# Kernel optimization log

Measured on AMD Instinct MI355X. Metric: run time of the kernel, lower is better.

The kernel has to match this reference:

```python
import jax, jax.numpy as jnp
import numpy as np

D = 1280          # hidden_size
NH = 16           # num_heads
HD = 80           # head_dim
DEPTH = 4         # number of vision blocks
INTER = 3420      # mlp intermediate size
MERGE = 2         # spatial_merge_size
OUT = 3584        # merger out_hidden_size
GRID = (1, 40, 40)  # (t, h, w) patch grid -> 1600 tokens
N = GRID[0] * GRID[1] * GRID[2]
PATCH_IN = 3 * 2 * 14 * 14  # in_channels * temporal_patch * patch^2 = 1176


def _pos_emb():
    """Deterministic vision RoPE cos/sin per Qwen2_5_VLVisionModel.rot_pos_emb."""
    t, h, w = GRID
    mh, mw = h // MERGE, w // MERGE
    intra = np.arange(MERGE)
    row = np.arange(mh)[:, None, None, None] * MERGE + intra[None, None, :, None]
    col = np.arange(mw)[None, :, None, None] * MERGE + intra[None, None, None, :]
    row = np.broadcast_to(row, (mh, mw, MERGE, MERGE)).reshape(-1)
    col = np.broadcast_to(col, (mh, mw, MERGE, MERGE)).reshape(-1)
    pos = np.stack([row, col], axis=-1)        # (h*w, 2)
    if t > 1:
        pos = np.tile(pos, (t, 1))
    rot_dim = HD // 2                          # 40
    inv = 1.0 / (10000.0 ** (np.arange(0, rot_dim, 2, dtype=np.float64) / rot_dim))
    table = np.outer(np.arange(max(h, w)), inv)        # (max_hw, rot_dim//2)
    rpe = table[pos].reshape(pos.shape[0], -1)         # (N, rot_dim)
    emb = np.concatenate([rpe, rpe], axis=-1)          # (N, HD)
    return np.cos(emb).astype(np.float32), np.sin(emb).astype(np.float32)


def setup_inputs() -> dict:
    key = jax.random.key(0)
    ks = iter(jax.random.split(key, 40))
    def w(shape, s=0.02):
        return jax.random.normal(next(ks), shape, jnp.float32) * s
    cos, sin = _pos_emb()
    return dict(
        pixel_values=w((N, PATCH_IN), 1.0),
        cos=jnp.asarray(cos), sin=jnp.asarray(sin),
        patch_w=w((D, PATCH_IN)),                       # Conv3d stride==kernel -> linear
        norm1_w=jnp.ones((DEPTH, D), jnp.float32),
        qkv_w=w((DEPTH, 3 * D, D)), qkv_b=jnp.zeros((DEPTH, 3 * D), jnp.float32),
        proj_w=w((DEPTH, D, D)), proj_b=jnp.zeros((DEPTH, D), jnp.float32),
        norm2_w=jnp.ones((DEPTH, D), jnp.float32),
        gate_w=w((DEPTH, INTER, D)), gate_b=jnp.zeros((DEPTH, INTER), jnp.float32),
        up_w=w((DEPTH, INTER, D)), up_b=jnp.zeros((DEPTH, INTER), jnp.float32),
        down_w=w((DEPTH, D, INTER)), down_b=jnp.zeros((DEPTH, D), jnp.float32),
        lnq_w=jnp.ones((D,), jnp.float32),
        m1_w=w((D * MERGE ** 2, D * MERGE ** 2)), m1_b=jnp.zeros((D * MERGE ** 2,), jnp.float32),
        m2_w=w((OUT, D * MERGE ** 2)), m2_b=jnp.zeros((OUT,), jnp.float32),
    )


def _rms(x, w, eps=1e-6):
    return x * jax.lax.rsqrt(jnp.mean(x * x, axis=-1, keepdims=True) + eps) * w


def _rotate_half(x):
    x1, x2 = jnp.split(x, 2, axis=-1)
    return jnp.concatenate([-x2, x1], axis=-1)


def _forward(pixel_values, cos, sin, patch_w, norm1_w, qkv_w, qkv_b, proj_w, proj_b,
             norm2_w, gate_w, gate_b, up_w, up_b, down_w, down_b,
             lnq_w, m1_w, m1_b, m2_w, m2_b):
    # patch embed: Conv3d with kernel==stride collapses to a linear projection
    x = pixel_values @ patch_w.T                       # (N, D)
    c = cos[:, None, :]                                # (N, 1, HD)
    s = sin[:, None, :]
    scale = HD ** -0.5
    for i in range(DEPTH):
        # --- attention ---
        h = _rms(x, norm1_w[i])
        qkv = (h @ qkv_w[i].T + qkv_b[i]).reshape(N, 3, NH, HD)
        q, k, v = qkv[:, 0], qkv[:, 1], qkv[:, 2]      # (N, NH, HD)
        q = q * c + _rotate_half(q) * s
        k = k * c + _rotate_half(k) * s
        # NOTE: this impl applies NO cu_seqlens window mask -> full dense attention
        aw = jnp.einsum('nhd,mhd->hnm', q, k) * scale  # (NH, N, N)
        aw = jax.nn.softmax(aw.astype(jnp.float32), axis=-1).astype(x.dtype)
        o = jnp.einsum('hnm,mhd->nhd', aw, v).reshape(N, D)
        x = x + o @ proj_w[i].T + proj_b[i]
        # --- mlp (SwiGLU) ---
        h = _rms(x, norm2_w[i])
        g = h @ gate_w[i].T + gate_b[i]
        u = h @ up_w[i].T + up_b[i]
        x = x + (jax.nn.silu(g) * u) @ down_w[i].T + down_b[i]
    # --- patch merger ---
    h = _rms(x, lnq_w).reshape(-1, D * MERGE ** 2)      # (N/4, 5120)
    h = jax.nn.gelu(h @ m1_w.T + m1_b, approximate=False)
    return h @ m2_w.T + m2_b                            # (N/4, OUT)


def reference(pixel_values, cos, sin, patch_w, norm1_w, qkv_w, qkv_b, proj_w, proj_b,
              norm2_w, gate_w, gate_b, up_w, up_b, down_w, down_b,
              lnq_w, m1_w, m1_b, m2_w, m2_b):
    return _forward(pixel_values, cos, sin, patch_w, norm1_w, qkv_w, qkv_b, proj_w,
                    proj_b, norm2_w, gate_w, gate_b, up_w, up_b, down_w, down_b,
                    lnq_w, m1_w, m1_b, m2_w, m2_b)
```

## Files before the change

### kernel.cpp

```cpp
#include <hip/hip_runtime.h>


typedef __bf16 bf16x8 __attribute__((ext_vector_type(8)));
typedef float  f32x4  __attribute__((ext_vector_type(4)));
typedef unsigned short u16;

#define DEV __device__ __forceinline__

DEV u16 f2bf(float f) {
    union { float f; unsigned u; } v; v.f = f;
    unsigned r = v.u + 0x7FFFu + ((v.u >> 16) & 1u);
    return (u16)(r >> 16);
}
DEV float bf2f(u16 b) {
    union { float f; unsigned u; } v; v.u = ((unsigned)b) << 16; return v.f;
}

DEV void gload16(const u16* g, u16* l) {
    __builtin_amdgcn_global_load_lds(
        (const __attribute__((address_space(1))) unsigned int*)g,
        (__attribute__((address_space(3))) unsigned int*)l, 16, 0, 0);
}

enum { EPI_NONE = 0, EPI_BIAS = 1, EPI_BIAS_RESID = 2, EPI_BIAS_GELU = 3, EPI_PART = 4 };

DEV unsigned xcd_map(unsigned lin, unsigned nwg) {
    unsigned q = nwg >> 3, r = nwg & 7, xc = lin & 7, off = lin >> 3;
    return (xc < r ? xc * (q + 1) : r * (q + 1) + (xc - r) * q) + off;
}

__global__ void cvt_kernel(const float* __restrict__ src, u16* __restrict__ dst,
                           int Rs, int Cs, int Rp, int Cp,
                           long long sls, long long dls)
{
    const float* s = src + (size_t)blockIdx.y * sls;
    u16* d = dst + (size_t)blockIdx.y * dls;
    int idx = blockIdx.x * 256 + threadIdx.x;
    int cpc = Cp >> 3;
    if (idx >= Rp * cpc) return;
    int row = idx / cpc;
    int c0  = (idx - row * cpc) * 8;
    u16 v[8];
    if (row < Rs && c0 + 8 <= Cs) {
        float4 a = *reinterpret_cast<const float4*>(&s[(size_t)row * Cs + c0]);
        float4 b = *reinterpret_cast<const float4*>(&s[(size_t)row * Cs + c0 + 4]);
        v[0] = f2bf(a.x); v[1] = f2bf(a.y); v[2] = f2bf(a.z); v[3] = f2bf(a.w);
        v[4] = f2bf(b.x); v[5] = f2bf(b.y); v[6] = f2bf(b.z); v[7] = f2bf(b.w);
    } else {
#pragma unroll
        for (int j = 0; j < 8; ++j) {
            int c = c0 + j;
            v[j] = (row < Rs && c < Cs) ? f2bf(s[(size_t)row * Cs + c]) : (u16)0;
        }
    }
    *reinterpret_cast<uint4*>(&d[(size_t)row * Cp + c0]) =
        *reinterpret_cast<const uint4*>(v);
}

__global__ void gub_kernel(const float* __restrict__ gb, const float* __restrict__ ub,
                           float* __restrict__ dst)
{
    int i = blockIdx.x * 256 + threadIdx.x;
    if (i >= 4 * 6912) return;
    int l = i / 6912, c = i - l * 6912;
    float v = 0.f;
    if (c < 3456) { if (c < 3420) v = gb[l * 3420 + c]; }
    else { int c2 = c - 3456; if (c2 < 3420) v = ub[l * 3420 + c2]; }
    dst[i] = v;
}

template <int EPI, bool OF32>
__global__ __launch_bounds__(256, 3)
void gemm16_kernel(const u16* __restrict__ A, const u16* __restrict__ B,
                   const float* __restrict__ bias, const float* __restrict__ resid,
                   void* __restrict__ outp, int Kp, int ldc, int Rlim,
                   int ktn, size_t zstride)
{
    __shared__ u16 sA[3][4096];
    __shared__ u16 sB[3][4096];
    const int tid  = threadIdx.x;
    const int lane = tid & 63;
    const int w    = tid >> 6;

    const unsigned gy  = gridDim.y;
    const unsigned nwg = gridDim.x * gy;
    const unsigned lin = blockIdx.x + blockIdx.y * gridDim.x;
    const unsigned id2 = xcd_map(lin, nwg);
    const int c0 = (int)(id2 / gy) * 128;
    const int r0 = (int)(id2 - (id2 / gy) * gy) * 128;

    const int wr  = (w >> 1) * 64;
    const int wc  = (w & 1) * 64;
    const int l15 = lane & 15;
    const int kk  = (lane >> 4) * 8;
    const int pco = (((lane >> 4) ^ ((l15 >> 1) & 3)) * 8) - kk;

    const int ca  = w * 128 + lane;
    const int cb  = ca + 64;
    const int sza = ((ca & 3) ^ ((ca >> 3) & 3)) * 8;
    const int szb = ((cb & 3) ^ ((cb >> 3) & 3)) * 8;
    const size_t arow0 = (size_t)(r0 + (ca >> 2)) * Kp + sza;
    const size_t brow0 = (size_t)(c0 + (ca >> 2)) * Kp + sza;
    const size_t arow1 = (size_t)(r0 + (cb >> 2)) * Kp + szb;
    const size_t brow1 = (size_t)(c0 + (cb >> 2)) * Kp + szb;

    f32x4 acc[4][4];
#pragma unroll
    for (int i = 0; i < 4; ++i)
#pragma unroll
        for (int j = 0; j < 4; ++j) acc[i][j] = (f32x4){0.f, 0.f, 0.f, 0.f};

    const int kt0 = blockIdx.z * ktn;
    auto stage = [&](int kt, int buf) {
        int k0 = kt * 32;
        gload16(A + arow0 + k0, &sA[buf][ca * 8]);
        gload16(B + brow0 + k0, &sB[buf][ca * 8]);
        gload16(A + arow1 + k0, &sA[buf][cb * 8]);
        gload16(B + brow1 + k0, &sB[buf][cb * 8]);
    };
    auto compute = [&](int buf) {
        bf16x8 af[4], bfr[4];
#pragma unroll
        for (int f = 0; f < 4; ++f) {
            af[f]  = *reinterpret_cast<const bf16x8*>(&sA[buf][(wr + f * 16 + l15) * 32 + kk + pco]);
            bfr[f] = *reinterpret_cast<const bf16x8*>(&sB[buf][(wc + f * 16 + l15) * 32 + kk + pco]);
        }
#pragma unroll
        for (int fr = 0; fr < 4; ++fr)
#pragma unroll
            for (int fc = 0; fc < 4; ++fc)
                acc[fr][fc] = __builtin_amdgcn_mfma_f32_16x16x32_bf16(af[fr], bfr[fc], acc[fr][fc], 0, 0, 0);
    };

    const int NT = ktn;
    stage(kt0, 0);
    if (NT > 1) stage(kt0 + 1, 1);
    int bcur = 0;
    for (int t = 0; t < NT - 1; ++t) {
        asm volatile("s_waitcnt vmcnt(4)" ::: "memory");
        __builtin_amdgcn_s_barrier();
        __builtin_amdgcn_sched_barrier(0);
        if (t + 2 < NT) {
            int bn = bcur + 2; if (bn >= 3) bn -= 3;
            stage(kt0 + t + 2, bn);
        }
        __builtin_amdgcn_sched_barrier(0);
        compute(bcur);
        bcur = (bcur == 2) ? 0 : bcur + 1;
    }
    asm volatile("s_waitcnt vmcnt(0)" ::: "memory");
    __builtin_amdgcn_s_barrier();
    __builtin_amdgcn_sched_barrier(0);
    compute(bcur);

    const int rowb = r0 + wr + (lane >> 4) * 4;
    const int colb = c0 + wc + l15;
    if (EPI == EPI_PART) {
        float* pp = (float*)outp + (size_t)blockIdx.z * zstride;
#pragma unroll
        for (int fc = 0; fc < 4; ++fc) {
            int col = colb + fc * 16;
#pragma unroll
            for (int fr = 0; fr < 4; ++fr)
#pragma unroll
                for (int r2 = 0; r2 < 4; ++r2)
                    pp[(size_t)(rowb + fr * 16 + r2) * ldc + col] = acc[fr][fc][r2];
        }
        return;
    }
#pragma unroll
    for (int fc = 0; fc < 4; ++fc) {
        int col = colb + fc * 16;
        float bv = (EPI != EPI_NONE) ? bias[col] : 0.f;
#pragma unroll
        for (int fr = 0; fr < 4; ++fr) {
#pragma unroll
            for (int r2 = 0; r2 < 4; ++r2) {
                int row = rowb + fr * 16 + r2;
                if (row >= Rlim) continue;
                float v = acc[fr][fc][r2] + bv;
                if (EPI == EPI_BIAS_RESID) v += resid[(size_t)row * ldc + col];
                if (EPI == EPI_BIAS_GELU)  v = 0.5f * v * (1.f + erff(v * 0.70710678118f));
                if (OF32) ((float*)outp)[(size_t)row * ldc + col] = v;
                else      ((u16*)outp)[(size_t)row * ldc + col] = f2bf(v);
            }
        }
    }
}

template <int EPI, bool OF32>
__global__ __launch_bounds__(256, 4)
void gemm64_kernel(const u16* __restrict__ A, const u16* __restrict__ B,
                   const float* __restrict__ bias, const float* __restrict__ resid,
                   void* __restrict__ outp, int Kp, int ldc, int Rlim)
{
    __shared__ u16 sA[3][2048];
    __shared__ u16 sB[3][4096];
    const int tid  = threadIdx.x;
    const int lane = tid & 63;
    const int w    = tid >> 6;

    const unsigned gy  = gridDim.y;
    const unsigned nwg = gridDim.x * gy;
    const unsigned lin = blockIdx.x + blockIdx.y * gridDim.x;
    const unsigned id2 = xcd_map(lin, nwg);
    const int c0 = (int)(id2 / gy) * 128;
    const int r0 = (int)(id2 - (id2 / gy) * gy) * 64;

    const int wr  = (w >> 1) * 32;
    const int wc  = (w & 1) * 64;
    const int l15 = lane & 15;
    const int kk  = (lane >> 4) * 8;
    const int pco = (((lane >> 4) ^ ((l15 >> 1) & 3)) * 8) - kk;

    const int cB0 = tid, cB1 = tid + 256, cA = tid;
    const size_t bsrc0 = (size_t)(c0 + (cB0 >> 2)) * Kp + ((cB0 & 3) ^ ((cB0 >> 3) & 3)) * 8;
    const size_t bsrc1 = (size_t)(c0 + (cB1 >> 2)) * Kp + ((cB1 & 3) ^ ((cB1 >> 3) & 3)) * 8;
    const size_t asrc  = (size_t)(r0 + (cA  >> 2)) * Kp + ((cA  & 3) ^ ((cA  >> 3) & 3)) * 8;

    f32x4 acc[2][4];
#pragma unroll
    for (int i = 0; i < 2; ++i)
#pragma unroll
        for (int j = 0; j < 4; ++j) acc[i][j] = (f32x4){0.f, 0.f, 0.f, 0.f};

    auto stage = [&](int kt, int buf) {
        int k0 = kt * 32;
        gload16(B + bsrc0 + k0, &sB[buf][cB0 * 8]);
        gload16(B + bsrc1 + k0, &sB[buf][cB1 * 8]);
        gload16(A + asrc  + k0, &sA[buf][cA * 8]);
    };
    auto compute = [&](int buf) {
        bf16x8 af[2], bfr[4];
#pragma unroll
        for (int f = 0; f < 2; ++f)
            af[f]  = *reinterpret_cast<const bf16x8*>(&sA[buf][(wr + f * 16 + l15) * 32 + kk + pco]);
#pragma unroll
        for (int f = 0; f < 4; ++f)
            bfr[f] = *reinterpret_cast<const bf16x8*>(&sB[buf][(wc + f * 16 + l15) * 32 + kk + pco]);
#pragma unroll
        for (int fr = 0; fr < 2; ++fr)
#pragma unroll
            for (int fc = 0; fc < 4; ++fc)
                acc[fr][fc] = __builtin_amdgcn_mfma_f32_16x16x32_bf16(af[fr], bfr[fc], acc[fr][fc], 0, 0, 0);
    };

    const int NT = Kp >> 5;
    stage(0, 0);
    stage(1, 1);
    int bcur = 0;
    for (int t = 0; t < NT - 1; ++t) {
        asm volatile("s_waitcnt vmcnt(3)" ::: "memory");
        __builtin_amdgcn_s_barrier();
        __builtin_amdgcn_sched_barrier(0);
        if (t + 2 < NT) {
            int bn = bcur + 2; if (bn >= 3) bn -= 3;
            stage(t + 2, bn);
        }
        __builtin_amdgcn_sched_barrier(0);
        compute(bcur);
        bcur = (bcur == 2) ? 0 : bcur + 1;
    }
    asm volatile("s_waitcnt vmcnt(0)" ::: "memory");
    __builtin_amdgcn_s_barrier();
    __builtin_amdgcn_sched_barrier(0);
    compute(bcur);

    const int rowb = r0 + wr + (lane >> 4) * 4;
    const int colb = c0 + wc + l15;
#pragma unroll
    for (int fc = 0; fc < 4; ++fc) {
        int col = colb + fc * 16;
        float bv = (EPI != EPI_NONE) ? bias[col] : 0.f;
#pragma unroll
        for (int fr = 0; fr < 2; ++fr) {
#pragma unroll
            for (int r2 = 0; r2 < 4; ++r2) {
                int row = rowb + fr * 16 + r2;
                if (row >= Rlim) continue;
                float v = acc[fr][fc][r2] + bv;
                if (EPI == EPI_BIAS_RESID) v += resid[(size_t)row * ldc + col];
                if (EPI == EPI_BIAS_GELU)  v = 0.5f * v * (1.f + erff(v * 0.70710678118f));
                if (OF32) ((float*)outp)[(size_t)row * ldc + col] = v;
                else      ((u16*)outp)[(size_t)row * ldc + col] = f2bf(v);
            }
        }
    }
}

template <int EPI, bool OF32>
__global__ __launch_bounds__(256, 4)
void gemm32_kernel(const u16* __restrict__ A, const u16* __restrict__ B,
                   const float* __restrict__ bias, const float* __restrict__ resid,
                   void* __restrict__ outp, int Kp, int ldc, int Rlim)
{
    __shared__ u16 sA[3][1024];
    __shared__ u16 sB[3][4096];
    const int tid  = threadIdx.x;
    const int lane = tid & 63;
    const int w    = tid >> 6;

    const unsigned gy  = gridDim.y;
    const unsigned nwg = gridDim.x * gy;
    const unsigned lin = blockIdx.x + blockIdx.y * gridDim.x;
    const unsigned id2 = xcd_map(lin, nwg);
    const int c0 = (int)(id2 / gy) * 128;
    const int r0 = (int)(id2 - (id2 / gy) * gy) * 32;

    const int wc  = w * 32;
    const int l15 = lane & 15;
    const int kk  = (lane >> 4) * 8;
    const int pco = (((lane >> 4) ^ ((l15 >> 1) & 3)) * 8) - kk;

    const int cB0 = tid, cB1 = tid + 256, cA = tid & 127;
    const size_t bsrc0 = (size_t)(c0 + (cB0 >> 2)) * Kp + ((cB0 & 3) ^ ((cB0 >> 3) & 3)) * 8;
    const size_t bsrc1 = (size_t)(c0 + (cB1 >> 2)) * Kp + ((cB1 & 3) ^ ((cB1 >> 3) & 3)) * 8;
    const size_t asrc  = (size_t)(r0 + (cA  >> 2)) * Kp + ((cA  & 3) ^ ((cA  >> 3) & 3)) * 8;

    f32x4 acc[2][2];
#pragma unroll
    for (int i = 0; i < 2; ++i)
#pragma unroll
        for (int j = 0; j < 2; ++j) acc[i][j] = (f32x4){0.f, 0.f, 0.f, 0.f};

    auto stage = [&](int kt, int buf) {
        int k0 = kt * 32;
        gload16(B + bsrc0 + k0, &sB[buf][cB0 * 8]);
        gload16(B + bsrc1 + k0, &sB[buf][cB1 * 8]);
        gload16(A + asrc  + k0, &sA[buf][cA * 8]);
    };
    auto compute = [&](int buf) {
        bf16x8 af[2], bfr[2];
#pragma unroll
        for (int f = 0; f < 2; ++f) {
            af[f]  = *reinterpret_cast<const bf16x8*>(&sA[buf][(f * 16 + l15) * 32 + kk + pco]);
            bfr[f] = *reinterpret_cast<const bf16x8*>(&sB[buf][(wc + f * 16 + l15) * 32 + kk + pco]);
        }
#pragma unroll
        for (int fr = 0; fr < 2; ++fr)
#pragma unroll
            for (int fc = 0; fc < 2; ++fc)
                acc[fr][fc] = __builtin_amdgcn_mfma_f32_16x16x32_bf16(af[fr], bfr[fc], acc[fr][fc], 0, 0, 0);
    };

    const int NT = Kp >> 5;
    stage(0, 0);
    stage(1, 1);
    int bcur = 0;
    for (int t = 0; t < NT - 1; ++t) {
        asm volatile("s_waitcnt vmcnt(3)" ::: "memory");
        __builtin_amdgcn_s_barrier();
        __builtin_amdgcn_sched_barrier(0);
        if (t + 2 < NT) {
            int bn = bcur + 2; if (bn >= 3) bn -= 3;
            stage(t + 2, bn);
        }
        __builtin_amdgcn_sched_barrier(0);
        compute(bcur);
        bcur = (bcur == 2) ? 0 : bcur + 1;
    }
    asm volatile("s_waitcnt vmcnt(0)" ::: "memory");
    __builtin_amdgcn_s_barrier();
    __builtin_amdgcn_sched_barrier(0);
    compute(bcur);

    const int rowb = r0 + (lane >> 4) * 4;
    const int colb = c0 + wc + l15;
#pragma unroll
    for (int fc = 0; fc < 2; ++fc) {
        int col = colb + fc * 16;
        float bv = (EPI != EPI_NONE) ? bias[col] : 0.f;
#pragma unroll
        for (int fr = 0; fr < 2; ++fr) {
#pragma unroll
            for (int r2 = 0; r2 < 4; ++r2) {
                int row = rowb + fr * 16 + r2;
                if (row >= Rlim) continue;
                float v = acc[fr][fc][r2] + bv;
                if (EPI == EPI_BIAS_RESID) v += resid[(size_t)row * ldc + col];
                if (EPI == EPI_BIAS_GELU)  v = 0.5f * v * (1.f + erff(v * 0.70710678118f));
                if (OF32) ((float*)outp)[(size_t)row * ldc + col] = v;
                else      ((u16*)outp)[(size_t)row * ldc + col] = f2bf(v);
            }
        }
    }
}

template <int GELU, bool OF32>
__global__ void reduce_kernel(const float* __restrict__ part, const float* __restrict__ bias,
                              void* __restrict__ outp, int C, int S, size_t zstride, int total4)
{
    int i = blockIdx.x * 256 + threadIdx.x;
    if (i >= total4) return;
    int cq = C >> 2;
    int rr = i / cq;
    int cc = (i - rr * cq) * 4;
    size_t bidx = (size_t)rr * C + cc;
    float4 s = *reinterpret_cast<const float4*>(&part[bidx]);
    for (int z = 1; z < S; ++z) {
        float4 p = *reinterpret_cast<const float4*>(&part[z * zstride + bidx]);
        s.x += p.x; s.y += p.y; s.z += p.z; s.w += p.w;
    }
    float4 b = *reinterpret_cast<const float4*>(&bias[cc]);
    s.x += b.x; s.y += b.y; s.z += b.z; s.w += b.w;
    if (GELU) {
        s.x = 0.5f * s.x * (1.f + erff(s.x * 0.70710678118f));
        s.y = 0.5f * s.y * (1.f + erff(s.y * 0.70710678118f));
        s.z = 0.5f * s.z * (1.f + erff(s.z * 0.70710678118f));
        s.w = 0.5f * s.w * (1.f + erff(s.w * 0.70710678118f));
    }
    if (OF32) {
        *reinterpret_cast<float4*>(&((float*)outp)[bidx]) = s;
    } else {
        u16 v[4] = { f2bf(s.x), f2bf(s.y), f2bf(s.z), f2bf(s.w) };
        *reinterpret_cast<uint2*>(&((u16*)outp)[bidx]) = *reinterpret_cast<const uint2*>(v);
    }
}

__global__ void rms_kernel(const float* __restrict__ x, const float* __restrict__ w,
                           u16* __restrict__ out, int cols)
{
    const int row = blockIdx.x;
    const int tid = threadIdx.x;
    const float* xr = x + (size_t)row * cols;
    float ss = 0.f;
    for (int c = tid; c < cols; c += 256) { float v = xr[c]; ss += v * v; }
#pragma unroll
    for (int m = 1; m < 64; m <<= 1) ss += __shfl_xor(ss, m);
    __shared__ float wsum[4];
    if ((tid & 63) == 0) wsum[tid >> 6] = ss;
    __syncthreads();
    float tot = wsum[0] + wsum[1] + wsum[2] + wsum[3];
    float rs = rsqrtf(tot / (float)cols + 1e-6f);
    u16* orow = out + (size_t)row * cols;
    for (int c = tid; c < cols; c += 256) orow[c] = f2bf(xr[c] * rs * w[c]);
}

__global__ void rope_kernel(u16* __restrict__ qkv, const float* __restrict__ cosb,
                            const float* __restrict__ sinb)
{
    int idx = blockIdx.x * 256 + threadIdx.x;
    int n   = idx / 640;
    int rem = idx - n * 640;
    int hh  = rem / 40;
    int d   = rem - hh * 40;
    float c0 = cosb[n * 80 + d];
    float s0 = sinb[n * 80 + d];
    float c1 = cosb[n * 80 + d + 40];
    float s1 = sinb[n * 80 + d + 40];
    size_t base = (size_t)n * 3840 + hh * 80;
    float a = bf2f(qkv[base + d]), b = bf2f(qkv[base + d + 40]);
    qkv[base + d]      = f2bf(a * c0 - b * s0);
    qkv[base + d + 40] = f2bf(b * c1 + a * s1);
    base += 1280;
    a = bf2f(qkv[base + d]); b = bf2f(qkv[base + d + 40]);
    qkv[base + d]      = f2bf(a * c0 - b * s0);
    qkv[base + d + 40] = f2bf(b * c1 + a * s1);
}

__global__ void silu_mul_kernel(const u16* __restrict__ gu, u16* __restrict__ outb)
{
    int idx = blockIdx.x * 256 + threadIdx.x;
    if (idx >= 1664 * 432) return;
    int row = idx / 432, c8 = (idx - row * 432) * 8;
    u16 gv[8], uv[8];
    *reinterpret_cast<uint4*>(gv) = *reinterpret_cast<const uint4*>(&gu[(size_t)row * 6912 + c8]);
    *reinterpret_cast<uint4*>(uv) = *reinterpret_cast<const uint4*>(&gu[(size_t)row * 6912 + 3456 + c8]);
#pragma unroll
    for (int j = 0; j < 8; ++j) {
        float x = bf2f(gv[j]);
        gv[j] = f2bf(x / (1.f + __expf(-x)) * bf2f(uv[j]));
    }
    *reinterpret_cast<uint4*>(&outb[(size_t)row * 3456 + c8]) = *reinterpret_cast<const uint4*>(gv);
}

__global__ __launch_bounds__(256, 2)
void attn_kernel(const u16* __restrict__ qkv, u16* __restrict__ o)
{
    __shared__ __align__(16) u16      Klds[2][64][104];
    __shared__ __align__(16) unsigned Vt32[2][80][36];
    __shared__ __align__(16) u16      Plds[4][16][72];
    const int tid  = threadIdx.x;
    const int lane = tid & 63;
    const int w    = tid >> 6;
    const int l15  = lane & 15;
    const int kk   = (lane >> 4) * 8;
    unsigned lin = blockIdx.y * 25 + blockIdx.x;
    unsigned id2 = (lin & 7) * 50 + (lin >> 3);
    const int hh = (int)(id2 / 25);
    const int qt = (int)(id2 - hh * 25);
    const float scale = 0.11180339887498949f;

    const int koff = 1280 + hh * 80;
    const int voff = 2560 + hh * 80;

    {
        int r  = tid >> 2;
        int cq = 80 + (tid & 3) * 4;
        *reinterpret_cast<uint2*>(&Klds[0][r][cq]) = make_uint2(0u, 0u);
        *reinterpret_cast<uint2*>(&Klds[1][r][cq]) = make_uint2(0u, 0u);
    }

    const int qrow = qt * 64 + w * 16 + l15;
    bf16x8 aq[3];
#pragma unroll
    for (int s = 0; s < 3; ++s) {
        int d = 32 * s + kk;
        union { bf16x8 v; uint4 q; } uu;
        if (d < 80) uu.q = *reinterpret_cast<const uint4*>(&qkv[(size_t)qrow * 3840 + hh * 80 + d]);
        else        uu.q = make_uint4(0u, 0u, 0u, 0u);
        aq[s] = uu.v;
    }

    const int kc0 = tid, kc1 = tid + 256, kc2 = tid + 512;
    const int kr0 = kc0 / 10, k80 = (kc0 - kr0 * 10) * 8;
    const int kr1 = kc1 / 10, k81 = (kc1 - kr1 * 10) * 8;
    const int kr2 = kc2 / 10, k82 = (kc2 - kr2 * 10) * 8;
    const size_t ksrc0 = (size_t)kr0 * 3840 + koff + k80;
    const size_t ksrc1 = (size_t)kr1 * 3840 + koff + k81;
    const size_t ksrc2 = (size_t)kr2 * 3840 + koff + k82;
    const int rpA = tid & 31, gA = tid >> 5;
    const int gB = 8 + (tid >> 5);
    const size_t vsrcA = (size_t)(2 * rpA) * 3840 + voff + gA * 8;
    const size_t vsrcB = (size_t)(2 * rpA) * 3840 + voff + gB * 8;

    uint4 kg0, kg1, kg2, va0, va1, vb0, vb1;
    auto LOADR = [&](int kb) {
        size_t tb = (size_t)kb * 245760;
        kg0 = *reinterpret_cast<const uint4*>(&qkv[tb + ksrc0]);
        kg1 = *reinterpret_cast<const uint4*>(&qkv[tb + ksrc1]);
        if (tid < 128) kg2 = *reinterpret_cast<const uint4*>(&qkv[tb + ksrc2]);
        va0 = *reinterpret_cast<const uint4*>(&qkv[tb + vsrcA]);
        va1 = *reinterpret_cast<const uint4*>(&qkv[tb + vsrcA + 3840]);
        if (tid < 64) {
            vb0 = *reinterpret_cast<const uint4*>(&qkv[tb + vsrcB]);
            vb1 = *reinterpret_cast<const uint4*>(&qkv[tb + vsrcB + 3840]);
        }
    };
    auto STORE = [&](int b) {
        *reinterpret_cast<uint4*>(&Klds[b][kr0][k80]) = kg0;
        *reinterpret_cast<uint4*>(&Klds[b][kr1][k81]) = kg1;
        if (tid < 128) *reinterpret_cast<uint4*>(&Klds[b][kr2][k82]) = kg2;
        union { uint4 q; u16 h[8]; } xa0, xa1;
        xa0.q = va0; xa1.q = va1;
#pragma unroll
        for (int j = 0; j < 8; ++j)
            Vt32[b][gA * 8 + j][rpA] = (unsigned)xa0.h[j] | ((unsigned)xa1.h[j] << 16);
        if (tid < 64) {
            union { uint4 q; u16 h[8]; } xb0, xb1;
            xb0.q = vb0; xb1.q = vb1;
#pragma unroll
            for (int j = 0; j < 8; ++j)
                Vt32[b][gB * 8 + j][rpA] = (unsigned)xb0.h[j] | ((unsigned)xb1.h[j] << 16);
        }
    };

    f32x4 acc_o[5];
#pragma unroll
    for (int fd = 0; fd < 5; ++fd) acc_o[fd] = (f32x4){0.f, 0.f, 0.f, 0.f};
    float m[4], lsum[4];
#pragma unroll
    for (int r2 = 0; r2 < 4; ++r2) { m[r2] = -__builtin_inff(); lsum[r2] = 0.f; }

    LOADR(0);
    STORE(0);
    __syncthreads();
    int cur = 0;

    for (int kb = 0; kb < 25; ++kb) {
        if (kb < 24) LOADR(kb + 1);

        f32x4 sf[4];
#pragma unroll
        for (int fc = 0; fc < 4; ++fc) {
            f32x4 c = (f32x4){0.f, 0.f, 0.f, 0.f};
#pragma unroll
            for (int s = 0; s < 3; ++s)
                c = __builtin_amdgcn_mfma_f32_16x16x32_bf16(
                        aq[s],
                        *reinterpret_cast<const bf16x8*>(&Klds[cur][fc * 16 + l15][32 * s + kk]),
                        c, 0, 0, 0);
            sf[fc] = c * scale;
        }

        float mx[4];
#pragma unroll
        for (int r2 = 0; r2 < 4; ++r2)
            mx[r2] = fmaxf(fmaxf(sf[0][r2], sf[1][r2]), fmaxf(sf[2][r2], sf[3][r2]));
#pragma unroll
        for (int msk = 1; msk <= 8; msk <<= 1)
#pragma unroll
            for (int r2 = 0; r2 < 4; ++r2)
                mx[r2] = fmaxf(mx[r2], __shfl_xor(mx[r2], msk));
        float alpha[4];
#pragma unroll
        for (int r2 = 0; r2 < 4; ++r2) {
            float mn = fmaxf(m[r2], mx[r2]);
            alpha[r2] = __expf(m[r2] - mn);
            m[r2] = mn;
        }
        float psum[4] = {0.f, 0.f, 0.f, 0.f};
#pragma unroll
        for (int fc = 0; fc < 4; ++fc)
#pragma unroll
            for (int r2 = 0; r2 < 4; ++r2) {
                float p = __expf(sf[fc][r2] - m[r2]);
                sf[fc][r2] = p;
                psum[r2] += p;
            }
#pragma unroll
        for (int msk = 1; msk <= 8; msk <<= 1)
#pragma unroll
            for (int r2 = 0; r2 < 4; ++r2) psum[r2] += __shfl_xor(psum[r2], msk);
#pragma unroll
        for (int r2 = 0; r2 < 4; ++r2) lsum[r2] = lsum[r2] * alpha[r2] + psum[r2];
#pragma unroll
        for (int fd = 0; fd < 5; ++fd)
#pragma unroll
            for (int r2 = 0; r2 < 4; ++r2) acc_o[fd][r2] *= alpha[r2];

        const int prow = (lane >> 4) * 4;
#pragma unroll
        for (int fc = 0; fc < 4; ++fc)
#pragma unroll
            for (int r2 = 0; r2 < 4; ++r2)
                Plds[w][prow + r2][fc * 16 + l15] = f2bf(sf[fc][r2]);

        bf16x8 ap[2];
#pragma unroll
        for (int ks = 0; ks < 2; ++ks)
            ap[ks] = *reinterpret_cast<const bf16x8*>(&Plds[w][l15][32 * ks + kk]);
#pragma unroll
        for (int fd = 0; fd < 5; ++fd) {
            const u16* vrow = reinterpret_cast<const u16*>(&Vt32[cur][fd * 16 + l15][0]);
#pragma unroll
            for (int ks = 0; ks < 2; ++ks)
                acc_o[fd] = __builtin_amdgcn_mfma_f32_16x16x32_bf16(
                        ap[ks],
                        *reinterpret_cast<const bf16x8*>(&vrow[32 * ks + kk]),
                        acc_o[fd], 0, 0, 0);
        }

        if (kb < 24) STORE(cur ^ 1);
        __syncthreads();
        cur ^= 1;
    }

    float inv[4];
#pragma unroll
    for (int r2 = 0; r2 < 4; ++r2) inv[r2] = 1.f / lsum[r2];
    const int orow = qt * 64 + w * 16 + (lane >> 4) * 4;
    const int ocol = hh * 80 + l15;
#pragma unroll
    for (int fd = 0; fd < 5; ++fd)
#pragma unroll
        for (int r2 = 0; r2 < 4; ++r2)
            o[(size_t)(orow + r2) * 1280 + ocol + fd * 16] = f2bf(acc_o[fd][r2] * inv[r2]);
}

extern "C" void kernel_launch(void* const* d_in, const int* in_sizes, int n_in,
                              void* d_out, int out_size, void* d_ws, size_t ws_size,
                              hipStream_t stream)
{
    const float* pixel  = (const float*)d_in[0];
    const float* cosb   = (const float*)d_in[1];
    const float* sinb   = (const float*)d_in[2];
    const float* patchw = (const float*)d_in[3];
    const float* n1w    = (const float*)d_in[4];
    const float* qkvw   = (const float*)d_in[5];
    const float* qkvb   = (const float*)d_in[6];
    const float* projw  = (const float*)d_in[7];
    const float* projb  = (const float*)d_in[8];
    const float* n2w    = (const float*)d_in[9];
    const float* gatew  = (const float*)d_in[10];
    const float* gateb  = (const float*)d_in[11];
    const float* upw    = (const float*)d_in[12];
    const float* upb    = (const float*)d_in[13];
    const float* downw  = (const float*)d_in[14];
    const float* downb  = (const float*)d_in[15];
    const float* lnqw   = (const float*)d_in[16];
    const float* m1w    = (const float*)d_in[17];
    const float* m1b    = (const float*)d_in[18];
    const float* m2w    = (const float*)d_in[19];
    const float* m2b    = (const float*)d_in[20];
    float* out = (float*)d_out;

    char* base = (char*)d_ws;
    float* x      = (float*)(base);
    u16*   h      = (u16*)(base + 8519680);
    u16*   qbuf   = (u16*)(base + 12779520);
    u16*   pix16  = qbuf;
    u16*   gsep   = (u16*)(base + 25559040);
    u16*   o      = gsep;
    u16*   pw16   = gsep;
    u16*   gu     = (u16*)(base + 37060608);
    u16*   t1     = gu;
    float* guB    = (float*)(base + 60063744);
    u16*   qkvw16 = (u16*)(base + 60174336);
    u16*   projw16= (u16*)(base + 99495936);
    u16*   guw16  = (u16*)(base + 112603136);
    u16*   downw16= (u16*)(base + 183382016);
    u16*   m1w16  = guw16;
    u16*   m2w16  = (u16*)(base + 112603136 + 52428800);
    float* part   = (float*)qkvw16;

    dim3 blk(256);
    auto cvb = [](int Rp, int Cp) { return (Rp * (Cp >> 3) + 255) / 256; };

    cvt_kernel<<<dim3(cvb(1664,1216),1), blk, 0, stream>>>(pixel, pix16, 1600, 1176, 1664, 1216, 0, 0);
    cvt_kernel<<<dim3(cvb(1280,1216),1), blk, 0, stream>>>(patchw, pw16, 1280, 1176, 1280, 1216, 0, 0);
    cvt_kernel<<<dim3(cvb(15360,1280),1), blk, 0, stream>>>(qkvw, qkvw16, 15360, 1280, 15360, 1280, 0, 0);
    cvt_kernel<<<dim3(cvb(5120,1280),1), blk, 0, stream>>>(projw, projw16, 5120, 1280, 5120, 1280, 0, 0);
    cvt_kernel<<<dim3(cvb(3456,1280),4), blk, 0, stream>>>(gatew, guw16, 3420, 1280, 3456, 1280, 4377600LL, 8847360LL);
    cvt_kernel<<<dim3(cvb(3456,1280),4), blk, 0, stream>>>(upw, guw16 + 4423680, 3420, 1280, 3456, 1280, 4377600LL, 8847360LL);
    cvt_kernel<<<dim3(cvb(1280,3456),4), blk, 0, stream>>>(downw, downw16, 1280, 3420, 1280, 3456, 4377600LL, 4423680LL);
    gub_kernel<<<108, blk, 0, stream>>>(gateb, upb, guB);

    gemm32_kernel<EPI_NONE, true><<<dim3(10,52), blk, 0, stream>>>(pix16, pw16, nullptr, nullptr, x, 1216, 1280, 1664);
    for (int i = 0; i < 4; ++i) {
        rms_kernel<<<1600, blk, 0, stream>>>(x, n1w + i*1280, h, 1280);
        gemm64_kernel<EPI_BIAS, false><<<dim3(30,26), blk, 0, stream>>>(h, qkvw16 + (size_t)i*4915200, qkvb + i*3840, nullptr, qbuf, 1280, 3840, 1664);
        rope_kernel<<<4000, blk, 0, stream>>>(qbuf, cosb, sinb);
        attn_kernel<<<dim3(25,16), blk, 0, stream>>>(qbuf, o);
        gemm32_kernel<EPI_BIAS_RESID, true><<<dim3(10,52), blk, 0, stream>>>(o, projw16 + (size_t)i*1638400, projb + i*1280, x, x, 1280, 1280, 1664);
        rms_kernel<<<1600, blk, 0, stream>>>(x, n2w + i*1280, h, 1280);
        gemm16_kernel<EPI_BIAS, false><<<dim3(54,13), blk, 0, stream>>>(h, guw16 + (size_t)i*8847360, guB + i*6912, nullptr, gu, 1280, 6912, 1664, 40, 0);
        silu_mul_kernel<<<2808, blk, 0, stream>>>(gu, gsep);
        gemm32_kernel<EPI_BIAS_RESID, true><<<dim3(10,52), blk, 0, stream>>>(gsep, downw16 + (size_t)i*4423680, downb + i*1280, x, x, 3456, 1280, 1664);
    }
    cvt_kernel<<<dim3(cvb(5120,5120),1), blk, 0, stream>>>(m1w, m1w16, 5120, 5120, 5120, 5120, 0, 0);
    cvt_kernel<<<dim3(cvb(3584,5120),1), blk, 0, stream>>>(m2w, m2w16, 3584, 5120, 3584, 5120, 0, 0);
    rms_kernel<<<1600, blk, 0, stream>>>(x, lnqw, h, 1280);
    gemm16_kernel<EPI_PART, false><<<dim3(40,4,5), blk, 0, stream>>>(h, m1w16, nullptr, nullptr, part, 5120, 5120, 512, 32, 2621440);
    reduce_kernel<1, false><<<2560, blk, 0, stream>>>(part, m1b, t1, 5120, 5, 2621440, 655360);
    gemm16_kernel<EPI_PART, false><<<dim3(28,4,5), blk, 0, stream>>>(t1, m2w16, nullptr, nullptr, part, 5120, 3584, 512, 32, 1835008);
    reduce_kernel<0, true><<<1400, blk, 0, stream>>>(part, m2b, out, 3584, 5, 1835008, 358400);
}
```

Measured before the change: 1.293 ms.

## Shrink attention blocks to 2 waves over 32 query rows and merge weight conversions

The attention kernel now runs 128-thread blocks, each covering 32 query rows with two wavefronts, and the grid doubles to 800 blocks. The aim is to fill more of the GPU and raise occupancy, at the cost of loading each K/V tile twice as often per query. The seven fp32-to-bf16 weight conversion launches are folded into one kernel and the two merger conversions into another, which cuts launch overhead.

```diff
diff --git a/kernel.cpp b/kernel.cpp
--- a/kernel.cpp
+++ b/kernel.cpp
@@ -29,15 +29,10 @@
     return (xc < r ? xc * (q + 1) : r * (q + 1) + (xc - r) * q) + off;
 }
 
-__global__ void cvt_kernel(const float* __restrict__ src, u16* __restrict__ dst,
-                           int Rs, int Cs, int Rp, int Cp,
-                           long long sls, long long dls)
-{
-    const float* s = src + (size_t)blockIdx.y * sls;
-    u16* d = dst + (size_t)blockIdx.y * dls;
-    int idx = blockIdx.x * 256 + threadIdx.x;
+DEV void cvt_chunk(const float* __restrict__ s, u16* __restrict__ d,
+                   int idx, int Rs, int Cs, int Cp)
+{
     int cpc = Cp >> 3;
-    if (idx >= Rp * cpc) return;
     int row = idx / cpc;
     int c0  = (idx - row * cpc) * 8;
     u16 v[8];
@@ -55,6 +50,48 @@
     }
     *reinterpret_cast<uint4*>(&d[(size_t)row * Cp + c0]) =
         *reinterpret_cast<const uint4*>(v);
+}
+
+__global__ void cvtall_kernel(const float* __restrict__ pixel, const float* __restrict__ patchw,
+                              const float* __restrict__ qkvw,  const float* __restrict__ projw,
+                              const float* __restrict__ gatew, const float* __restrict__ upw,
+                              const float* __restrict__ downw,
+                              u16* pix16, u16* pw16, u16* qkvw16, u16* projw16,
+                              u16* guw16, u16* downw16)
+{
+    int idx = blockIdx.x * 256 + threadIdx.x;
+    const int C0 = 252928, C1 = 447488, C2 = 2905088, C3 = 3724288;
+    const int C4 = 5936128, C5 = 8147968, C6 = 10359808;
+    if (idx < C0) {
+        cvt_chunk(pixel, pix16, idx, 1600, 1176, 1216);
+    } else if (idx < C1) {
+        cvt_chunk(patchw, pw16, idx - C0, 1280, 1176, 1216);
+    } else if (idx < C2) {
+        cvt_chunk(qkvw, qkvw16, idx - C1, 15360, 1280, 1280);
+    } else if (idx < C3) {
+        cvt_chunk(projw, projw16, idx - C2, 5120, 1280, 1280);
+    } else if (idx < C4) {
+        int loc = idx - C3; int l = loc / 552960; int wi = loc - l * 552960;
+        cvt_chunk(gatew + (size_t)l * 4377600, guw16 + (size_t)l * 8847360,
+                  wi, 3420, 1280, 1280);
+    } else if (idx < C5) {
+        int loc = idx - C4; int l = loc / 552960; int wi = loc - l * 552960;
+        cvt_chunk(upw + (size_t)l * 4377600, guw16 + (size_t)l * 8847360 + 4423680,
+                  wi, 3420, 1280, 1280);
+    } else if (idx < C6) {
+        int loc = idx - C5; int l = loc / 552960; int wi = loc - l * 552960;
+        cvt_chunk(downw + (size_t)l * 4377600, downw16 + (size_t)l * 4423680,
+                  wi, 1280, 3420, 3456);
+    }
+}
+
+__global__ void cvtmm_kernel(const float* __restrict__ m1w, const float* __restrict__ m2w,
+                             u16* m1w16, u16* m2w16)
+{
+    int idx = blockIdx.x * 256 + threadIdx.x;
+    const int N7 = 3276800;
+    if (idx < N7) cvt_chunk(m1w, m1w16, idx, 5120, 5120, 5120);
+    else if (idx < N7 + 2293760) cvt_chunk(m2w, m2w16, idx - N7, 3584, 5120, 5120);
 }
 
 __global__ void gub_kernel(const float* __restrict__ gb, const float* __restrict__ ub,
@@ -474,34 +511,34 @@
     *reinterpret_cast<uint4*>(&outb[(size_t)row * 3456 + c8]) = *reinterpret_cast<const uint4*>(gv);
 }
 
-__global__ __launch_bounds__(256, 2)
+__global__ __launch_bounds__(128, 4)
 void attn_kernel(const u16* __restrict__ qkv, u16* __restrict__ o)
 {
     __shared__ __align__(16) u16      Klds[2][64][104];
     __shared__ __align__(16) unsigned Vt32[2][80][36];
-    __shared__ __align__(16) u16      Plds[4][16][72];
+    __shared__ __align__(16) u16      Plds[2][16][72];
     const int tid  = threadIdx.x;
     const int lane = tid & 63;
     const int w    = tid >> 6;
     const int l15  = lane & 15;
     const int kk   = (lane >> 4) * 8;
-    unsigned lin = blockIdx.y * 25 + blockIdx.x;
-    unsigned id2 = (lin & 7) * 50 + (lin >> 3);
-    const int hh = (int)(id2 / 25);
-    const int qt = (int)(id2 - hh * 25);
+    unsigned lin = blockIdx.y * 50 + blockIdx.x;
+    unsigned id2 = (lin & 7) * 100 + (lin >> 3);
+    const int hh = (int)(id2 / 50);
+    const int qt = (int)(id2 - hh * 50);
     const float scale = 0.11180339887498949f;
 
     const int koff = 1280 + hh * 80;
     const int voff = 2560 + hh * 80;
 
     {
-        int r  = tid >> 2;
-        int cq = 80 + (tid & 3) * 4;
-        *reinterpret_cast<uint2*>(&Klds[0][r][cq]) = make_uint2(0u, 0u);
-        *reinterpret_cast<uint2*>(&Klds[1][r][cq]) = make_uint2(0u, 0u);
-    }
-
-    const int qrow = qt * 64 + w * 16 + l15;
+        int r = tid >> 1;
+        int cq = 80 + (tid & 1) * 8;
+        *reinterpret_cast<uint4*>(&Klds[0][r][cq]) = make_uint4(0u, 0u, 0u, 0u);
+        *reinterpret_cast<uint4*>(&Klds[1][r][cq]) = make_uint4(0u, 0u, 0u, 0u);
+    }
+
+    const int qrow = qt * 32 + w * 16 + l15;
     bf16x8 aq[3];
 #pragma unroll
     for (int s = 0; s < 3; ++s) {
@@ -512,46 +549,55 @@
         aq[s] = uu.v;
     }
 
-    const int kc0 = tid, kc1 = tid + 256, kc2 = tid + 512;
-    const int kr0 = kc0 / 10, k80 = (kc0 - kr0 * 10) * 8;
-    const int kr1 = kc1 / 10, k81 = (kc1 - kr1 * 10) * 8;
-    const int kr2 = kc2 / 10, k82 = (kc2 - kr2 * 10) * 8;
-    const size_t ksrc0 = (size_t)kr0 * 3840 + koff + k80;
-    const size_t ksrc1 = (size_t)kr1 * 3840 + koff + k81;
-    const size_t ksrc2 = (size_t)kr2 * 3840 + koff + k82;
-    const int rpA = tid & 31, gA = tid >> 5;
-    const int gB = 8 + (tid >> 5);
-    const size_t vsrcA = (size_t)(2 * rpA) * 3840 + voff + gA * 8;
-    const size_t vsrcB = (size_t)(2 * rpA) * 3840 + voff + gB * 8;
-
-    uint4 kg0, kg1, kg2, va0, va1, vb0, vb1;
+    int kr[5], k8[5];
+    size_t ksrc[5];
+#pragma unroll
+    for (int i = 0; i < 5; ++i) {
+        int kc = tid + 128 * i;
+        kr[i] = kc / 10; k8[i] = (kc - kr[i] * 10) * 8;
+        ksrc[i] = (size_t)kr[i] * 3840 + koff + k8[i];
+    }
+    const int rpA = tid & 31;
+    const int g0 = tid >> 5;
+    const int g1 = 4 + g0;
+    const int g2 = 8 + (tid >> 5);
+    const size_t vs0 = (size_t)(2 * rpA) * 3840 + voff + g0 * 8;
+    const size_t vs1 = (size_t)(2 * rpA) * 3840 + voff + g1 * 8;
+    const size_t vs2 = (size_t)(2 * rpA) * 3840 + voff + g2 * 8;
+
+    uint4 kg[5], v00, v01, v10, v11, v20, v21;
     auto LOADR = [&](int kb) {
         size_t tb = (size_t)kb * 245760;
-        kg0 = *reinterpret_cast<const uint4*>(&qkv[tb + ksrc0]);
-        kg1 = *reinterpret_cast<const uint4*>(&qkv[tb + ksrc1]);
-        if (tid < 128) kg2 = *reinterpret_cast<const uint4*>(&qkv[tb + ksrc2]);
-        va0 = *reinterpret_cast<const uint4*>(&qkv[tb + vsrcA]);
-        va1 = *reinterpret_cast<const uint4*>(&qkv[tb + vsrcA + 3840]);
+#pragma unroll
+        for (int i = 0; i < 5; ++i)
+            kg[i] = *reinterpret_cast<const uint4*>(&qkv[tb + ksrc[i]]);
+        v00 = *reinterpret_cast<const uint4*>(&qkv[tb + vs0]);
+        v01 = *reinterpret_cast<const uint4*>(&qkv[tb + vs0 + 3840]);
+        v10 = *reinterpret_cast<const uint4*>(&qkv[tb + vs1]);
+        v11 = *reinterpret_cast<const uint4*>(&qkv[tb + vs1 + 3840]);
         if (tid < 64) {
-            vb0 = *reinterpret_cast<const uint4*>(&qkv[tb + vsrcB]);
-            vb1 = *reinterpret_cast<const uint4*>(&qkv[tb + vsrcB + 3840]);
+            v20 = *reinterpret_cast<const uint4*>(&qkv[tb + vs2]);
+            v21 = *reinterpret_cast<const uint4*>(&qkv[tb + vs2 + 3840]);
         }
     };
     auto STORE = [&](int b) {
-        *reinterpret_cast<uint4*>(&Klds[b][kr0][k80]) = kg0;
-        *reinterpret_cast<uint4*>(&Klds[b][kr1][k81]) = kg1;
-        if (tid < 128) *reinterpret_cast<uint4*>(&Klds[b][kr2][k82]) = kg2;
-        union { uint4 q; u16 h[8]; } xa0, xa1;
-        xa0.q = va0; xa1.q = va1;
+#pragma unroll
+        for (int i = 0; i < 5; ++i)
+            *reinterpret_cast<uint4*>(&Klds[b][kr[i]][k8[i]]) = kg[i];
+        union { uint4 q; u16 h[8]; } x0, x1;
+        x0.q = v00; x1.q = v01;
 #pragma unroll
         for (int j = 0; j < 8; ++j)
-            Vt32[b][gA * 8 + j][rpA] = (unsigned)xa0.h[j] | ((unsigned)xa1.h[j] << 16);
+            Vt32[b][g0 * 8 + j][rpA] = (unsigned)x0.h[j] | ((unsigned)x1.h[j] << 16);
+        x0.q = v10; x1.q = v11;
+#pragma unroll
+        for (int j = 0; j < 8; ++j)
+            Vt32[b][g1 * 8 + j][rpA] = (unsigned)x0.h[j] | ((unsigned)x1.h[j] << 16);
         if (tid < 64) {
-            union { uint4 q; u16 h[8]; } xb0, xb1;
-            xb0.q = vb0; xb1.q = vb1;
+            x0.q = v20; x1.q = v21;
 #pragma unroll
             for (int j = 0; j < 8; ++j)
-                Vt32[b][gB * 8 + j][rpA] = (unsigned)xb0.h[j] | ((unsigned)xb1.h[j] << 16);
+                Vt32[b][g2 * 8 + j][rpA] = (unsigned)x0.h[j] | ((unsigned)x1.h[j] << 16);
         }
     };
 
@@ -649,7 +695,7 @@
     float inv[4];
 #pragma unroll
     for (int r2 = 0; r2 < 4; ++r2) inv[r2] = 1.f / lsum[r2];
-    const int orow = qt * 64 + w * 16 + (lane >> 4) * 4;
+    const int orow = qt * 32 + w * 16 + (lane >> 4) * 4;
     const int ocol = hh * 80 + l15;
 #pragma unroll
     for (int fd = 0; fd < 5; ++fd)
@@ -705,15 +751,9 @@
     float* part   = (float*)qkvw16;
 
     dim3 blk(256);
-    auto cvb = [](int Rp, int Cp) { return (Rp * (Cp >> 3) + 255) / 256; };
-
-    cvt_kernel<<<dim3(cvb(1664,1216),1), blk, 0, stream>>>(pixel, pix16, 1600, 1176, 1664, 1216, 0, 0);
-    cvt_kernel<<<dim3(cvb(1280,1216),1), blk, 0, stream>>>(patchw, pw16, 1280, 1176, 1280, 1216, 0, 0);
-    cvt_kernel<<<dim3(cvb(15360,1280),1), blk, 0, stream>>>(qkvw, qkvw16, 15360, 1280, 15360, 1280, 0, 0);
-    cvt_kernel<<<dim3(cvb(5120,1280),1), blk, 0, stream>>>(projw, projw16, 5120, 1280, 5120, 1280, 0, 0);
-    cvt_kernel<<<dim3(cvb(3456,1280),4), blk, 0, stream>>>(gatew, guw16, 3420, 1280, 3456, 1280, 4377600LL, 8847360LL);
-    cvt_kernel<<<dim3(cvb(3456,1280),4), blk, 0, stream>>>(upw, guw16 + 4423680, 3420, 1280, 3456, 1280, 4377600LL, 8847360LL);
-    cvt_kernel<<<dim3(cvb(1280,3456),4), blk, 0, stream>>>(downw, downw16, 1280, 3420, 1280, 3456, 4377600LL, 4423680LL);
+
+    cvtall_kernel<<<40469, blk, 0, stream>>>(pixel, patchw, qkvw, projw, gatew, upw, downw,
+                                             pix16, pw16, qkvw16, projw16, guw16, downw16);
     gub_kernel<<<108, blk, 0, stream>>>(gateb, upb, guB);
 
     gemm32_kernel<EPI_NONE, true><<<dim3(10,52), blk, 0, stream>>>(pix16, pw16, nullptr, nullptr, x, 1216, 1280, 1664);
@@ -721,15 +761,14 @@
         rms_kernel<<<1600, blk, 0, stream>>>(x, n1w + i*1280, h, 1280);
         gemm64_kernel<EPI_BIAS, false><<<dim3(30,26), blk, 0, stream>>>(h, qkvw16 + (size_t)i*4915200, qkvb + i*3840, nullptr, qbuf, 1280, 3840, 1664);
         rope_kernel<<<4000, blk, 0, stream>>>(qbuf, cosb, sinb);
-        attn_kernel<<<dim3(25,16), blk, 0, stream>>>(qbuf, o);
+        attn_kernel<<<dim3(50,16), dim3(128), 0, stream>>>(qbuf, o);
         gemm32_kernel<EPI_BIAS_RESID, true><<<dim3(10,52), blk, 0, stream>>>(o, projw16 + (size_t)i*1638400, projb + i*1280, x, x, 1280, 1280, 1664);
         rms_kernel<<<1600, blk, 0, stream>>>(x, n2w + i*1280, h, 1280);
         gemm16_kernel<EPI_BIAS, false><<<dim3(54,13), blk, 0, stream>>>(h, guw16 + (size_t)i*8847360, guB + i*6912, nullptr, gu, 1280, 6912, 1664, 40, 0);
         silu_mul_kernel<<<2808, blk, 0, stream>>>(gu, gsep);
         gemm32_kernel<EPI_BIAS_RESID, true><<<dim3(10,52), blk, 0, stream>>>(gsep, downw16 + (size_t)i*4423680, downb + i*1280, x, x, 3456, 1280, 1664);
     }
-    cvt_kernel<<<dim3(cvb(5120,5120),1), blk, 0, stream>>>(m1w, m1w16, 5120, 5120, 5120, 5120, 0, 0);
-    cvt_kernel<<<dim3(cvb(3584,5120),1), blk, 0, stream>>>(m2w, m2w16, 3584, 5120, 3584, 5120, 0, 0);
+    cvtmm_kernel<<<21760, blk, 0, stream>>>(m1w, m2w, m1w16, m2w16);
     rms_kernel<<<1600, blk, 0, stream>>>(x, lnqw, h, 1280);
     gemm16_kernel<EPI_PART, false><<<dim3(40,4,5), blk, 0, stream>>>(h, m1w16, nullptr, nullptr, part, 5120, 5120, 512, 32, 2621440);
     reduce_kernel<1, false><<<2560, blk, 0, stream>>>(part, m1b, t1, 5120, 5, 2621440, 655360);
```

New measurement: 1.620 ms. 25.4% more time.
